# Kernel optimization log

Hardware: AMD Instinct MI355X
Metric: run time of the kernel (lower is better)

Reference implementation:

```python
import jax, jax.numpy as jnp
import numpy as np

B, H, S, D = 4, 16, 1024, 64
MAX_REL = 128
VOCAB = 2 * MAX_REL + 1  # relative-position vocabulary


def setup_inputs() -> dict:
    key = jax.random.key(0)
    k1, k2, k3, k4 = jax.random.split(key, 4)
    tensor = jax.random.normal(k1, (B, H, S, D), dtype=jnp.float32)
    rel_keys_emb = jax.random.normal(k2, (VOCAB, D), dtype=jnp.float32) * 0.02
    rel_values_emb = jax.random.normal(k3, (VOCAB, D), dtype=jnp.float32) * 0.02
    # nn.Parameter initialized xavier_uniform_ on shape (1, H, 1, 1)
    bias = jax.random.uniform(k4, (1, H, 1, 1), dtype=jnp.float32, minval=-1.0, maxval=1.0)
    return {
        "tensor": tensor,
        "rel_keys_emb": rel_keys_emb,
        "rel_values_emb": rel_values_emb,
        "bias": bias,
        "max_relative_position": MAX_REL,
    }


def reference(tensor, rel_keys_emb, rel_values_emb, bias, max_relative_position):
    # forward(tensor, is_key=True, transpose=False)
    seq_len = tensor.shape[2]
    r = jnp.arange(seq_len)
    dist = jnp.clip(r[None, :] - r[:, None], -max_relative_position, max_relative_position)
    idx = dist + max_relative_position          # [S, S] in [0, 2*max_rel]
    rel_emb = rel_keys_emb[idx]                 # [S, S, D] gathered table
    # original: [S, B*H, D] @ [S, D, S] -> [S, B*H, S] -> [B, H, S, S]
    scores = jnp.einsum('bhsd,std->bhst', tensor, rel_emb)
    return scores + bias
```

## Files before the change

### kernel.cpp

```cpp
#include <hip/hip_runtime.h>


constexpr int S_    = 1024;
constexpr int D_    = 64;
constexpr int VOC   = 257;
constexpr int BQ    = 32;
constexpr int ESTR  = 72;
constexpr int XSTR  = 68;
constexpr int CSTR  = 34;

__device__ __forceinline__ unsigned short f2bf(float x) {
  unsigned u = __float_as_uint(x);
  return (unsigned short)((u + 0x7fffu + ((u >> 16) & 1u)) >> 16);
}
__device__ __forceinline__ float bf2f(unsigned short h) {
  return __uint_as_float(((unsigned)h) << 16);
}

__global__ __launch_bounds__(256, 2)
void relpos_kernel(const float* __restrict__ tensor,
                   const float* __restrict__ relk,
                   const float* __restrict__ bias,
                   float* __restrict__ out) {
  __shared__ __align__(16) unsigned short E_lds[VOC * ESTR];
  __shared__ __align__(16) float          x_lds[BQ * XSTR];
  __shared__ __align__(8)  unsigned short c_lds[VOC * CSTR];

  const int tid   = threadIdx.x;
  const int bh    = blockIdx.x >> 5;
  const int chunk = blockIdx.x & 31;
  const int s0    = chunk * BQ;
  const int h     = bh & 15;

  for (int it = 0; it < 17; ++it) {
    int idx = tid + 256 * it;
    if (idx < VOC * (D_ / 4)) {
      int v = idx >> 4, dq = idx & 15;
      const float4 e4 = *reinterpret_cast<const float4*>(&relk[v * D_ + dq * 4]);
      unsigned lo = ((unsigned)f2bf(e4.y) << 16) | f2bf(e4.x);
      unsigned hi = ((unsigned)f2bf(e4.w) << 16) | f2bf(e4.z);
      *reinterpret_cast<uint2*>(&E_lds[v * ESTR + dq * 4]) = make_uint2(lo, hi);
    }
  }
  {
    const float* xg = tensor + (size_t)(bh * S_ + s0) * D_;
#pragma unroll
    for (int it = 0; it < 2; ++it) {
      int idx = tid + 256 * it;
      int r = idx >> 4, dq = idx & 15;
      float4 v4 = *reinterpret_cast<const float4*>(&xg[r * D_ + dq * 4]);
      *reinterpret_cast<float4*>(&x_lds[r * XSTR + dq * 4]) = v4;
    }
  }
  __syncthreads();

  const int ti = tid >> 5;
  const int tj = tid & 31;
  float acc[4][8];
#pragma unroll
  for (int a = 0; a < 4; ++a)
#pragma unroll
    for (int b = 0; b < 8; ++b) acc[a][b] = 0.f;

  for (int dq = 0; dq < 8; ++dq) {
    float xr[4][8];
#pragma unroll
    for (int rr = 0; rr < 4; ++rr) {
      float4 a4 = *reinterpret_cast<const float4*>(&x_lds[(4 * ti + rr) * XSTR + dq * 8]);
      float4 b4 = *reinterpret_cast<const float4*>(&x_lds[(4 * ti + rr) * XSTR + dq * 8 + 4]);
      xr[rr][0] = a4.x; xr[rr][1] = a4.y; xr[rr][2] = a4.z; xr[rr][3] = a4.w;
      xr[rr][4] = b4.x; xr[rr][5] = b4.y; xr[rr][6] = b4.z; xr[rr][7] = b4.w;
    }
#pragma unroll
    for (int k = 0; k < 8; ++k) {
      int v = 32 * k + tj;
      uint4 e = *reinterpret_cast<const uint4*>(&E_lds[v * ESTR + dq * 8]);
      float ef[8];
      ef[0] = __uint_as_float(e.x << 16);
      ef[1] = __uint_as_float(e.x & 0xffff0000u);
      ef[2] = __uint_as_float(e.y << 16);
      ef[3] = __uint_as_float(e.y & 0xffff0000u);
      ef[4] = __uint_as_float(e.z << 16);
      ef[5] = __uint_as_float(e.z & 0xffff0000u);
      ef[6] = __uint_as_float(e.w << 16);
      ef[7] = __uint_as_float(e.w & 0xffff0000u);
#pragma unroll
      for (int rr = 0; rr < 4; ++rr)
#pragma unroll
        for (int dd = 0; dd < 8; ++dd)
          acc[rr][k] = fmaf(xr[rr][dd], ef[dd], acc[rr][k]);
    }
  }
#pragma unroll
  for (int k = 0; k < 8; ++k) {
    int v = 32 * k + tj;
    unsigned p0 = ((unsigned)f2bf(acc[1][k]) << 16) | f2bf(acc[0][k]);
    unsigned p1 = ((unsigned)f2bf(acc[3][k]) << 16) | f2bf(acc[2][k]);
    unsigned* cp = reinterpret_cast<unsigned*>(&c_lds[v * CSTR + 4 * ti]);
    cp[0] = p0; cp[1] = p1;
  }
  if (tid < 32) {
    float a = 0.f;
#pragma unroll 8
    for (int d = 0; d < D_; ++d)
      a = fmaf(x_lds[tid * XSTR + d], bf2f(E_lds[256 * ESTR + d]), a);
    c_lds[256 * CSTR + tid] = f2bf(a);
  }
  __syncthreads();

  const float bv = bias[h];
  float* op = out + (size_t)(bh * S_ + s0) * S_;
  for (int rr = 0; rr < BQ; ++rr) {
    const int s = s0 + rr;
    float* orow = op + (size_t)rr * S_;
#pragma unroll
    for (int j = 0; j < 4; ++j) {
      int t = tid + 256 * j;
      int v = t - s + 128;
      v = v < 0 ? 0 : (v > 256 ? 256 : v);
      orow[t] = bf2f(c_lds[v * CSTR + rr]) + bv;
    }
  }
}

extern "C" void kernel_launch(void* const* d_in, const int* in_sizes, int n_in,
                              void* d_out, int out_size, void* d_ws, size_t ws_size,
                              hipStream_t stream) {
  const float* tensor = (const float*)d_in[0];
  const float* relk   = (const float*)d_in[1];
  const float* bias   = (const float*)d_in[3];
  float* out          = (float*)d_out;

  const int B = 4, H = 16;
  dim3 grid(B * H * (S_ / BQ));
  dim3 block(256);
  relpos_kernel<<<grid, block, 0, stream>>>(tensor, relk, bias, out);
}
```

Baseline: 75.80 us.

## Compute relative-position score table with bf16 MFMA and larger query tiles

Replaces the scalar FMA dot products between query rows and the relative-key table with bf16 MFMA 16x16x32 instructions, loading operands straight from global memory instead of staging them in LDS. Doubles the rows per block to 64 and raises the occupancy hint, and folds the bias into the table before bf16 rounding so the write-out loop only expands values. This aims to cut compute and LDS staging so the kernel approaches the output-write bandwidth limit. Bias is now added before rounding, which slightly changes numerics.

```diff
diff --git a/kernel.cpp b/kernel.cpp
--- a/kernel.cpp
+++ b/kernel.cpp
@@ -1,125 +1,100 @@
 #include <hip/hip_runtime.h>
+#include <hip/hip_bf16.h>
 
 
-constexpr int S_    = 1024;
-constexpr int D_    = 64;
-constexpr int VOC   = 257;
-constexpr int BQ    = 32;
-constexpr int ESTR  = 72;
-constexpr int XSTR  = 68;
-constexpr int CSTR  = 34;
+constexpr int S_   = 1024;
+constexpr int D_   = 64;
+constexpr int VOC  = 257;
+constexpr int BQ   = 64;
+constexpr int CSTR = 66;
+
+typedef __attribute__((ext_vector_type(8))) short short8;
+typedef __attribute__((ext_vector_type(4))) float f32x4;
 
 __device__ __forceinline__ unsigned short f2bf(float x) {
   unsigned u = __float_as_uint(x);
   return (unsigned short)((u + 0x7fffu + ((u >> 16) & 1u)) >> 16);
 }
-__device__ __forceinline__ float bf2f(unsigned short h) {
-  return __uint_as_float(((unsigned)h) << 16);
+
+__device__ __forceinline__ short8 pack8(float4 a, float4 b) {
+  short8 r;
+  r[0] = (short)f2bf(a.x); r[1] = (short)f2bf(a.y);
+  r[2] = (short)f2bf(a.z); r[3] = (short)f2bf(a.w);
+  r[4] = (short)f2bf(b.x); r[5] = (short)f2bf(b.y);
+  r[6] = (short)f2bf(b.z); r[7] = (short)f2bf(b.w);
+  return r;
 }
 
-__global__ __launch_bounds__(256, 2)
-void relpos_kernel(const float* __restrict__ tensor,
-                   const float* __restrict__ relk,
-                   const float* __restrict__ bias,
-                   float* __restrict__ out) {
-  __shared__ __align__(16) unsigned short E_lds[VOC * ESTR];
-  __shared__ __align__(16) float          x_lds[BQ * XSTR];
-  __shared__ __align__(8)  unsigned short c_lds[VOC * CSTR];
+__device__ __forceinline__ unsigned packpair(float lo, float hi) {
+  return (unsigned)f2bf(lo) | ((unsigned)f2bf(hi) << 16);
+}
 
-  const int tid   = threadIdx.x;
-  const int bh    = blockIdx.x >> 5;
-  const int chunk = blockIdx.x & 31;
-  const int s0    = chunk * BQ;
-  const int h     = bh & 15;
+__global__ __launch_bounds__(256, 4)
+void relpos_mfma(const float* __restrict__ tensor,
+                 const float* __restrict__ relk,
+                 const float* __restrict__ bias,
+                 float* __restrict__ out) {
+  __shared__ __align__(16) unsigned short c_lds[VOC * CSTR + 6];
 
-  for (int it = 0; it < 17; ++it) {
-    int idx = tid + 256 * it;
-    if (idx < VOC * (D_ / 4)) {
-      int v = idx >> 4, dq = idx & 15;
-      const float4 e4 = *reinterpret_cast<const float4*>(&relk[v * D_ + dq * 4]);
-      unsigned lo = ((unsigned)f2bf(e4.y) << 16) | f2bf(e4.x);
-      unsigned hi = ((unsigned)f2bf(e4.w) << 16) | f2bf(e4.z);
-      *reinterpret_cast<uint2*>(&E_lds[v * ESTR + dq * 4]) = make_uint2(lo, hi);
-    }
+  const int tid  = threadIdx.x;
+  const int lane = tid & 63;
+  const int w    = tid >> 6;
+  const int bh   = blockIdx.x >> 4;
+  const int s0   = (blockIdx.x & 15) * BQ;
+  const int h    = bh & 15;
+  const int l15  = lane & 15;
+  const int l4   = lane >> 4;
+
+  const float* xrow = tensor + ((size_t)(bh * S_ + s0 + 16 * w + l15)) * D_ + l4 * 8;
+  short8 a0, a1;
+  {
+    float4 p0 = *reinterpret_cast<const float4*>(xrow);
+    float4 p1 = *reinterpret_cast<const float4*>(xrow + 4);
+    a0 = pack8(p0, p1);
+    float4 q0 = *reinterpret_cast<const float4*>(xrow + 32);
+    float4 q1 = *reinterpret_cast<const float4*>(xrow + 36);
+    a1 = pack8(q0, q1);
   }
-  {
-    const float* xg = tensor + (size_t)(bh * S_ + s0) * D_;
-#pragma unroll
-    for (int it = 0; it < 2; ++it) {
-      int idx = tid + 256 * it;
-      int r = idx >> 4, dq = idx & 15;
-      float4 v4 = *reinterpret_cast<const float4*>(&xg[r * D_ + dq * 4]);
-      *reinterpret_cast<float4*>(&x_lds[r * XSTR + dq * 4]) = v4;
+
+  const float bv = bias[h];
+
+#pragma unroll 4
+  for (int nt = 0; nt < 17; ++nt) {
+    const int vrow = 16 * nt + l15;
+    const int erow = vrow > 256 ? 256 : vrow;
+    const float* ep = relk + (size_t)erow * D_ + l4 * 8;
+    float4 e00 = *reinterpret_cast<const float4*>(ep);
+    float4 e01 = *reinterpret_cast<const float4*>(ep + 4);
+    float4 e10 = *reinterpret_cast<const float4*>(ep + 32);
+    float4 e11 = *reinterpret_cast<const float4*>(ep + 36);
+    short8 b0 = pack8(e00, e01);
+    short8 b1 = pack8(e10, e11);
+
+    f32x4 acc = {0.f, 0.f, 0.f, 0.f};
+    acc = __builtin_amdgcn_mfma_f32_16x16x32_bf16(a0, b0, acc, 0, 0, 0);
+    acc = __builtin_amdgcn_mfma_f32_16x16x32_bf16(a1, b1, acc, 0, 0, 0);
+
+    if (vrow <= 256) {
+      const int row0 = 16 * w + l4 * 4;
+      unsigned* cp = reinterpret_cast<unsigned*>(&c_lds[vrow * CSTR + row0]);
+      cp[0] = packpair(acc[0] + bv, acc[1] + bv);
+      cp[1] = packpair(acc[2] + bv, acc[3] + bv);
     }
   }
   __syncthreads();
 
-  const int ti = tid >> 5;
-  const int tj = tid & 31;
-  float acc[4][8];
-#pragma unroll
-  for (int a = 0; a < 4; ++a)
-#pragma unroll
-    for (int b = 0; b < 8; ++b) acc[a][b] = 0.f;
-
-  for (int dq = 0; dq < 8; ++dq) {
-    float xr[4][8];
-#pragma unroll
-    for (int rr = 0; rr < 4; ++rr) {
-      float4 a4 = *reinterpret_cast<const float4*>(&x_lds[(4 * ti + rr) * XSTR + dq * 8]);
-      float4 b4 = *reinterpret_cast<const float4*>(&x_lds[(4 * ti + rr) * XSTR + dq * 8 + 4]);
-      xr[rr][0] = a4.x; xr[rr][1] = a4.y; xr[rr][2] = a4.z; xr[rr][3] = a4.w;
-      xr[rr][4] = b4.x; xr[rr][5] = b4.y; xr[rr][6] = b4.z; xr[rr][7] = b4.w;
-    }
-#pragma unroll
-    for (int k = 0; k < 8; ++k) {
-      int v = 32 * k + tj;
-      uint4 e = *reinterpret_cast<const uint4*>(&E_lds[v * ESTR + dq * 8]);
-      float ef[8];
-      ef[0] = __uint_as_float(e.x << 16);
-      ef[1] = __uint_as_float(e.x & 0xffff0000u);
-      ef[2] = __uint_as_float(e.y << 16);
-      ef[3] = __uint_as_float(e.y & 0xffff0000u);
-      ef[4] = __uint_as_float(e.z << 16);
-      ef[5] = __uint_as_float(e.z & 0xffff0000u);
-      ef[6] = __uint_as_float(e.w << 16);
-      ef[7] = __uint_as_float(e.w & 0xffff0000u);
-#pragma unroll
-      for (int rr = 0; rr < 4; ++rr)
-#pragma unroll
-        for (int dd = 0; dd < 8; ++dd)
-          acc[rr][k] = fmaf(xr[rr][dd], ef[dd], acc[rr][k]);
-    }
-  }
-#pragma unroll
-  for (int k = 0; k < 8; ++k) {
-    int v = 32 * k + tj;
-    unsigned p0 = ((unsigned)f2bf(acc[1][k]) << 16) | f2bf(acc[0][k]);
-    unsigned p1 = ((unsigned)f2bf(acc[3][k]) << 16) | f2bf(acc[2][k]);
-    unsigned* cp = reinterpret_cast<unsigned*>(&c_lds[v * CSTR + 4 * ti]);
-    cp[0] = p0; cp[1] = p1;
-  }
-  if (tid < 32) {
-    float a = 0.f;
-#pragma unroll 8
-    for (int d = 0; d < D_; ++d)
-      a = fmaf(x_lds[tid * XSTR + d], bf2f(E_lds[256 * ESTR + d]), a);
-    c_lds[256 * CSTR + tid] = f2bf(a);
-  }
-  __syncthreads();
-
-  const float bv = bias[h];
-  float* op = out + (size_t)(bh * S_ + s0) * S_;
+  float* orow = out + ((size_t)bh * S_ + (size_t)s0) * S_;
+  int vb = 128 - s0;
   for (int rr = 0; rr < BQ; ++rr) {
-    const int s = s0 + rr;
-    float* orow = op + (size_t)rr * S_;
 #pragma unroll
     for (int j = 0; j < 4; ++j) {
-      int t = tid + 256 * j;
-      int v = t - s + 128;
+      const int t = tid + 256 * j;
+      int v = t + vb;
       v = v < 0 ? 0 : (v > 256 ? 256 : v);
-      orow[t] = bf2f(c_lds[v * CSTR + rr]) + bv;
+      orow[t] = __uint_as_float(((unsigned)c_lds[v * CSTR + rr]) << 16);
     }
+    orow += S_;
+    --vb;
   }
 }
 
@@ -134,5 +109,5 @@
   const int B = 4, H = 16;
   dim3 grid(B * H * (S_ / BQ));
   dim3 block(256);
-  relpos_kernel<<<grid, block, 0, stream>>>(tensor, relk, bias, out);
+  relpos_mfma<<<grid, block, 0, stream>>>(tensor, relk, bias, out);
 }
```

After: 73.40 us. -3.2%, faster.
